# Performance work log

Measured on AMD Instinct MI355X. Metric: run time of the kernel, lower is better.

Reference implementation:

```python
import jax, jax.numpy as jnp
import numpy as np

N_NODES = 50000
N_EDGES = 800000
IN_DIM = 1024
HID = 512          # hidden_channels * heads, heads=1
N_CLASSES = 6
N_GRAPHS = 8
NEG_SLOPE = 0.2    # PyG GATConv default LeakyReLU slope
EPS = 1e-16


def gat_conv(x, W, att_src, att_dst, bias, src, dst):
    """PyG GATConv with heads=1, concat=True.
    x: [N, Fin], W: [Fin, C], att_src/att_dst: [C], bias: [C],
    src/dst: [E] (edge_index[0], edge_index[1]); messages flow src -> dst.
    """
    h = x @ W                                   # [N, C]
    a_s = h @ att_src                           # [N]
    a_d = h @ att_dst                           # [N]
    e = jax.nn.leaky_relu(a_s[src] + a_d[dst], NEG_SLOPE)   # [E]
    # segment softmax over destination node
    m = jax.ops.segment_max(e, dst, num_segments=N_NODES)   # [N]
    ex = jnp.exp(e - m[dst])                                 # [E]
    denom = jax.ops.segment_sum(ex, dst, num_segments=N_NODES)  # [N]
    alpha = ex / (denom[dst] + EPS)                           # [E]
    msg = alpha[:, None] * h[src]                             # [E, C]
    out = jax.ops.segment_sum(msg, dst, num_segments=N_NODES)  # [N, C]
    return out + bias


def setup_inputs() -> dict:
    key = jax.random.key(0)
    ks = jax.random.split(key, 20)
    x = jax.random.normal(ks[0], (N_NODES, IN_DIM), dtype=jnp.float32)
    edge_index = jax.random.randint(ks[1], (2, N_EDGES), 0, N_NODES, dtype=jnp.int32)
    batch = jnp.sort(jax.random.randint(ks[2], (N_NODES,), 0, N_GRAPHS, dtype=jnp.int32))

    def glorot(k, shape):
        fan = shape[0] + shape[-1]
        return jax.random.normal(k, shape, dtype=jnp.float32) * jnp.sqrt(2.0 / fan)

    inp = {"x": x, "edge_index": edge_index, "batch": batch}
    dims = [(IN_DIM, HID), (HID, HID), (HID, HID)]
    for i, (fi, fo) in enumerate(dims, start=1):
        inp[f"W{i}"] = glorot(ks[3 * i], (fi, fo))
        inp[f"as{i}"] = glorot(ks[3 * i + 1], (fo,))
        inp[f"ad{i}"] = glorot(ks[3 * i + 2], (fo,))
        inp[f"b{i}"] = jnp.zeros((fo,), dtype=jnp.float32)
    inp["Wlin"] = glorot(ks[13], (HID, N_CLASSES))
    inp["blin"] = jnp.zeros((N_CLASSES,), dtype=jnp.float32)
    return inp


def reference(x, W1, as1, ad1, b1, W2, as2, ad2, b2, W3, as3, ad3, b3,
              Wlin, blin, edge_index, batch):
    src, dst = edge_index[0], edge_index[1]
    h = gat_conv(x, W1, as1, ad1, b1, src, dst)
    h = jax.nn.relu(h)
    h = gat_conv(h, W2, as2, ad2, b2, src, dst)
    h = jax.nn.relu(h)
    h = gat_conv(h, W3, as3, ad3, b3, src, dst)
    # global_max_pool over graphs; dropout is identity in eval mode
    pooled = jax.ops.segment_max(h, batch, num_segments=N_GRAPHS)  # [G, HID]
    return pooled @ Wlin + blin                                     # [G, num_classes]
```

## Files before the change

### kernel.cpp

```cpp
#include <hip/hip_runtime.h>
#include <cmath>

#define N_NODES 50000
#define N_EDGES 800000
#define IN_DIM 1024
#define HID 512
#define N_CLASSES 6
#define N_GRAPHS 8
#define NEG_SLOPE 0.2f
#define SCAN_BLK 256
#define N_SCAN_BLOCKS ((N_NODES + SCAN_BLK - 1) / SCAN_BLK)
#define POOL_STRIP 256
#define POOL_NBLOCKS ((N_NODES + POOL_STRIP - 1) / POOL_STRIP)

typedef _Float16 half8 __attribute__((ext_vector_type(8)));
typedef float floatx4 __attribute__((ext_vector_type(4)));

__global__ __launch_bounds__(256) void transpose_cast_W(const float* __restrict__ W,
                                                        _Float16* __restrict__ Wt,
                                                        int K) {
    __shared__ float sh[32][33];
    const int kb = blockIdx.x * 32, nb = blockIdx.y * 32;
    const int tx = threadIdx.x & 31, ty = threadIdx.x >> 5;
#pragma unroll
    for (int i = 0; i < 32; i += 8)
        sh[ty + i][tx] = W[(size_t)(kb + ty + i) * HID + nb + tx];
    __syncthreads();
#pragma unroll
    for (int i = 0; i < 32; i += 8)
        Wt[(size_t)(nb + ty + i) * K + kb + tx] = (_Float16)sh[tx][ty + i];
}

__global__ __launch_bounds__(256) void gemm_mfma_f16(const float* __restrict__ A,
                                                     const _Float16* __restrict__ Bt,
                                                     _Float16* __restrict__ C,
                                                     int M, int K) {
    const int tid  = threadIdx.x;
    const int lane = tid & 63;
    const int wave = tid >> 6;
    const int wm = wave >> 1, wn = wave & 1;
    const int rowBase = blockIdx.y * 128;
    const int colBase = blockIdx.x * 128;

    __shared__ _Float16 As[128][40];
    __shared__ _Float16 Bs[128][40];

    const int srow  = tid >> 1;
    const int shalf = (tid & 1) * 16;

    const int fr = lane & 15;
    const int kc = lane >> 4;

    floatx4 acc[4][4] = {};

    int arow = rowBase + srow; if (arow >= M) arow = M - 1;
    const float*    aRow = A  + (size_t)arow * K + shalf;
    const _Float16* bRow = Bt + (size_t)(colBase + srow) * K + shalf;

    for (int kb = 0; kb < K; kb += 32) {
        const float* ap = aRow + kb;
        float4 af0 = *(const float4*)(ap + 0);
        float4 af1 = *(const float4*)(ap + 4);
        float4 af2 = *(const float4*)(ap + 8);
        float4 af3 = *(const float4*)(ap + 12);
        union { _Float16 h[16]; half8 v[2]; } au;
        au.h[0]  = (_Float16)af0.x; au.h[1]  = (_Float16)af0.y;
        au.h[2]  = (_Float16)af0.z; au.h[3]  = (_Float16)af0.w;
        au.h[4]  = (_Float16)af1.x; au.h[5]  = (_Float16)af1.y;
        au.h[6]  = (_Float16)af1.z; au.h[7]  = (_Float16)af1.w;
        au.h[8]  = (_Float16)af2.x; au.h[9]  = (_Float16)af2.y;
        au.h[10] = (_Float16)af2.z; au.h[11] = (_Float16)af2.w;
        au.h[12] = (_Float16)af3.x; au.h[13] = (_Float16)af3.y;
        au.h[14] = (_Float16)af3.z; au.h[15] = (_Float16)af3.w;
        half8* dstA = (half8*)&As[srow][shalf];
        const _Float16* bp = bRow + kb;
        half8 b0 = *(const half8*)bp;
        half8 b1 = *(const half8*)(bp + 8);
        half8* dstB = (half8*)&Bs[srow][shalf];
        dstA[0] = au.v[0]; dstA[1] = au.v[1];
        dstB[0] = b0;      dstB[1] = b1;
        __syncthreads();

        half8 afr[4], bfr[4];
#pragma unroll
        for (int mi = 0; mi < 4; ++mi)
            afr[mi] = *(const half8*)&As[wm * 64 + mi * 16 + fr][kc * 8];
#pragma unroll
        for (int ni = 0; ni < 4; ++ni)
            bfr[ni] = *(const half8*)&Bs[wn * 64 + ni * 16 + fr][kc * 8];
#pragma unroll
        for (int mi = 0; mi < 4; ++mi)
#pragma unroll
            for (int ni = 0; ni < 4; ++ni)
                acc[mi][ni] = __builtin_amdgcn_mfma_f32_16x16x32_f16(
                    afr[mi], bfr[ni], acc[mi][ni], 0, 0, 0);
        __syncthreads();
    }

#pragma unroll
    for (int mi = 0; mi < 4; ++mi) {
#pragma unroll
        for (int ni = 0; ni < 4; ++ni) {
            int col = colBase + wn * 64 + ni * 16 + fr;
#pragma unroll
            for (int j = 0; j < 4; ++j) {
                int row = rowBase + wm * 64 + mi * 16 + kc * 4 + j;
                if (row < M) C[(size_t)row * HID + col] = (_Float16)acc[mi][ni][j];
            }
        }
    }
}

__global__ __launch_bounds__(256) void adot_kernel(const _Float16* __restrict__ h,
                                                   const float* __restrict__ att_s,
                                                   const float* __restrict__ att_d,
                                                   float* __restrict__ a_s,
                                                   float* __restrict__ a_d) {
    int wave = threadIdx.x >> 6;
    int lane = threadIdx.x & 63;
    int n = blockIdx.x * 4 + wave;
    if (n >= N_NODES) return;
    half8 hv = *(const half8*)(h + (size_t)n * HID + lane * 8);
    float4 s0 = ((const float4*)att_s)[lane * 2];
    float4 s1 = ((const float4*)att_s)[lane * 2 + 1];
    float4 d0 = ((const float4*)att_d)[lane * 2];
    float4 d1 = ((const float4*)att_d)[lane * 2 + 1];
    float hf[8];
#pragma unroll
    for (int q = 0; q < 8; ++q) hf[q] = (float)hv[q];
    float ss = hf[0]*s0.x + hf[1]*s0.y + hf[2]*s0.z + hf[3]*s0.w
             + hf[4]*s1.x + hf[5]*s1.y + hf[6]*s1.z + hf[7]*s1.w;
    float sd = hf[0]*d0.x + hf[1]*d0.y + hf[2]*d0.z + hf[3]*d0.w
             + hf[4]*d1.x + hf[5]*d1.y + hf[6]*d1.z + hf[7]*d1.w;
#pragma unroll
    for (int off = 32; off; off >>= 1) {
        ss += __shfl_down(ss, off);
        sd += __shfl_down(sd, off);
    }
    if (lane == 0) { a_s[n] = ss; a_d[n] = sd; }
}

__global__ void count_kernel(const int* __restrict__ dst, int* __restrict__ cnt) {
    int i = blockIdx.x * blockDim.x + threadIdx.x;
    if (i < N_EDGES) atomicAdd(cnt + dst[i], 1);
}

__global__ __launch_bounds__(SCAN_BLK) void scan1_kernel(const int* __restrict__ cnt,
                                                         int* __restrict__ partial,
                                                         int* __restrict__ blocksum) {
    __shared__ int tmp[SCAN_BLK];
    int t = threadIdx.x;
    int i = blockIdx.x * SCAN_BLK + t;
    int v = (i < N_NODES) ? cnt[i] : 0;
    tmp[t] = v;
    __syncthreads();
    for (int off = 1; off < SCAN_BLK; off <<= 1) {
        int u = (t >= off) ? tmp[t - off] : 0;
        __syncthreads();
        tmp[t] += u;
        __syncthreads();
    }
    if (i < N_NODES) partial[i] = tmp[t] - v;
    if (t == SCAN_BLK - 1) blocksum[blockIdx.x] = tmp[t];
}

__global__ __launch_bounds__(SCAN_BLK) void scan2_kernel(int* __restrict__ blocksum) {
    __shared__ int tmp[SCAN_BLK];
    int t = threadIdx.x;
    int v = (t < N_SCAN_BLOCKS) ? blocksum[t] : 0;
    tmp[t] = v;
    __syncthreads();
    for (int off = 1; off < SCAN_BLK; off <<= 1) {
        int u = (t >= off) ? tmp[t - off] : 0;
        __syncthreads();
        tmp[t] += u;
        __syncthreads();
    }
    if (t < N_SCAN_BLOCKS) blocksum[t] = tmp[t] - v;
}

__global__ __launch_bounds__(SCAN_BLK) void scan3_kernel(const int* __restrict__ partial,
                                                         const int* __restrict__ blocksum,
                                                         int* __restrict__ rowptr,
                                                         int* __restrict__ cursor) {
    int i = blockIdx.x * SCAN_BLK + threadIdx.x;
    if (i < N_NODES) {
        int r = partial[i] + blocksum[blockIdx.x];
        rowptr[i] = r;
        cursor[i] = r;
    }
    if (i == 0) rowptr[N_NODES] = N_EDGES;
}

__global__ void scatter_kernel(const int* __restrict__ src, const int* __restrict__ dst,
                               int* __restrict__ cursor, int* __restrict__ src_s) {
    int i = blockIdx.x * blockDim.x + threadIdx.x;
    if (i >= N_EDGES) return;
    int p = atomicAdd(cursor + dst[i], 1);
    src_s[p] = src[i];
}

__global__ __launch_bounds__(256) void aggregate_fused(const int* __restrict__ rowptr,
                                                       const int* __restrict__ src_s,
                                                       const float* __restrict__ a_s,
                                                       const float* __restrict__ a_d,
                                                       const _Float16* __restrict__ h,
                                                       const float* __restrict__ bias,
                                                       int do_relu,
                                                       float* __restrict__ outx) {
    int wave = threadIdx.x >> 6;
    int lane = threadIdx.x & 63;
    int n = blockIdx.x * 4 + wave;
    if (n >= N_NODES) return;
    int beg = rowptr[n], end = rowptr[n + 1];
    float a_dn = a_d[n];
    float m = -__builtin_inff();
    float ssum = 0.f;
    float acc[8] = {};
    for (int j = beg; j < end; ++j) {
        int s = src_s[j];
        float v = a_s[s] + a_dn;
        v = v > 0.f ? v : NEG_SLOPE * v;
        float mn = fmaxf(m, v);
        float scale = __expf(m - mn);
        float p = __expf(v - mn);
        ssum = ssum * scale + p;
        m = mn;
        half8 hv = *(const half8*)(h + (size_t)s * HID + lane * 8);
#pragma unroll
        for (int q = 0; q < 8; ++q)
            acc[q] = fmaf(p, (float)hv[q], acc[q] * scale);
    }
    float inv = 1.f / (ssum + 1e-16f);
    const float4 b0 = ((const float4*)(bias + lane * 8))[0];
    const float4 b1 = ((const float4*)(bias + lane * 8))[1];
    float4 o0, o1;
    o0.x = acc[0] * inv + b0.x; o0.y = acc[1] * inv + b0.y;
    o0.z = acc[2] * inv + b0.z; o0.w = acc[3] * inv + b0.w;
    o1.x = acc[4] * inv + b1.x; o1.y = acc[5] * inv + b1.y;
    o1.z = acc[6] * inv + b1.z; o1.w = acc[7] * inv + b1.w;
    if (do_relu) {
        o0.x = fmaxf(o0.x, 0.f); o0.y = fmaxf(o0.y, 0.f);
        o0.z = fmaxf(o0.z, 0.f); o0.w = fmaxf(o0.w, 0.f);
        o1.x = fmaxf(o1.x, 0.f); o1.y = fmaxf(o1.y, 0.f);
        o1.z = fmaxf(o1.z, 0.f); o1.w = fmaxf(o1.w, 0.f);
    }
    float4* op = (float4*)(outx + (size_t)n * HID + lane * 8);
    op[0] = o0;
    op[1] = o1;
}

__global__ __launch_bounds__(128) void pool1_kernel(const float* __restrict__ X,
                                                    const int* __restrict__ batch,
                                                    float* __restrict__ partial) {
    const int t = threadIdx.x;
    const int b = blockIdx.x;
    const int n0 = b * POOL_STRIP;
    const int n1 = min(n0 + POOL_STRIP, N_NODES);
    const float NEG = -__builtin_inff();
    const float4 neg4 = make_float4(NEG, NEG, NEG, NEG);
#pragma unroll
    for (int g = 0; g < N_GRAPHS; ++g)
        ((float4*)(partial + ((size_t)b * N_GRAPHS + g) * HID))[t] = neg4;
    int gcur = batch[n0];
    float4 m = neg4;
    for (int n = n0; n < n1; ++n) {
        int g = batch[n];
        if (g != gcur) {
            ((float4*)(partial + ((size_t)b * N_GRAPHS + gcur) * HID))[t] = m;
            m = neg4;
            gcur = g;
        }
        float4 v = ((const float4*)(X + (size_t)n * HID))[t];
        m.x = fmaxf(m.x, v.x); m.y = fmaxf(m.y, v.y);
        m.z = fmaxf(m.z, v.z); m.w = fmaxf(m.w, v.w);
    }
    ((float4*)(partial + ((size_t)b * N_GRAPHS + gcur) * HID))[t] = m;
}

__global__ __launch_bounds__(128) void pool2_kernel(const float* __restrict__ partial,
                                                    float* __restrict__ pooled) {
    const int g = blockIdx.x;
    const int t = threadIdx.x;
    const float NEG = -__builtin_inff();
    float4 m = make_float4(NEG, NEG, NEG, NEG);
    for (int b = 0; b < POOL_NBLOCKS; ++b) {
        float4 v = ((const float4*)(partial + ((size_t)b * N_GRAPHS + g) * HID))[t];
        m.x = fmaxf(m.x, v.x); m.y = fmaxf(m.y, v.y);
        m.z = fmaxf(m.z, v.z); m.w = fmaxf(m.w, v.w);
    }
    ((float4*)(pooled + (size_t)g * HID))[t] = m;
}

__global__ __launch_bounds__(64) void final_linear_kernel(const float* __restrict__ pooled,
                                                          const float* __restrict__ Wlin,
                                                          const float* __restrict__ blin,
                                                          float* __restrict__ out) {
    int t = threadIdx.x;
    if (t >= N_GRAPHS * N_CLASSES) return;
    int g = t / N_CLASSES, c = t % N_CLASSES;
    float s = blin[c];
    for (int k = 0; k < HID; ++k)
        s = fmaf(pooled[(size_t)g * HID + k], Wlin[(size_t)k * N_CLASSES + c], s);
    out[t] = s;
}

extern "C" void kernel_launch(void* const* d_in, const int* in_sizes, int n_in,
                              void* d_out, int out_size, void* d_ws, size_t ws_size,
                              hipStream_t stream) {
    const float* x       = (const float*)d_in[0];
    const int*   eidx    = (const int*)d_in[1];
    const int*   batch   = (const int*)d_in[2];
    const float* W[3]    = {(const float*)d_in[3], (const float*)d_in[7], (const float*)d_in[11]};
    const float* Asrc[3] = {(const float*)d_in[4], (const float*)d_in[8], (const float*)d_in[12]};
    const float* Adst[3] = {(const float*)d_in[5], (const float*)d_in[9], (const float*)d_in[13]};
    const float* Bias[3] = {(const float*)d_in[6], (const float*)d_in[10], (const float*)d_in[14]};
    const float* Wlin    = (const float*)d_in[15];
    const float* blin    = (const float*)d_in[16];
    const int* src = eidx;
    const int* dst = eidx + N_EDGES;

    float* bufH   = (float*)d_ws;
    float* bufX   = bufH + (size_t)N_NODES * HID;
    float* a_s    = bufX + (size_t)N_NODES * HID;
    float* a_d    = a_s + N_NODES;
    float* pooled = a_d + N_NODES;
    int* cnt      = (int*)(pooled + N_GRAPHS * HID);
    int* rowptr   = cnt + N_NODES;
    int* cursor   = rowptr + N_NODES + 1;
    int* partial  = cursor + N_NODES;
    int* blocksum = partial + N_NODES;
    int* src_s    = blocksum + 256;
    _Float16* Wt  = (_Float16*)(src_s + N_EDGES);
    _Float16* hH  = (_Float16*)bufH;

    int edge_blocks = (N_EDGES + 255) / 256;

    hipMemsetAsync(cnt, 0, N_NODES * sizeof(int), stream);
    count_kernel<<<edge_blocks, 256, 0, stream>>>(dst, cnt);
    scan1_kernel<<<N_SCAN_BLOCKS, SCAN_BLK, 0, stream>>>(cnt, partial, blocksum);
    scan2_kernel<<<1, SCAN_BLK, 0, stream>>>(blocksum);
    scan3_kernel<<<N_SCAN_BLOCKS, SCAN_BLK, 0, stream>>>(partial, blocksum, rowptr, cursor);
    scatter_kernel<<<edge_blocks, 256, 0, stream>>>(src, dst, cursor, src_s);

    for (int l = 0; l < 3; ++l) {
        const float* Xin = (l == 0) ? x : bufX;
        int K = (l == 0) ? IN_DIM : HID;
        dim3 tgrid(K / 32, HID / 32);
        transpose_cast_W<<<tgrid, 256, 0, stream>>>(W[l], Wt, K);
        dim3 ggrid(HID / 128, (N_NODES + 127) / 128);
        gemm_mfma_f16<<<ggrid, 256, 0, stream>>>(Xin, Wt, hH, N_NODES, K);
        adot_kernel<<<(N_NODES + 3) / 4, 256, 0, stream>>>(hH, Asrc[l], Adst[l], a_s, a_d);
        aggregate_fused<<<(N_NODES + 3) / 4, 256, 0, stream>>>(
            rowptr, src_s, a_s, a_d, hH, Bias[l], (l < 2) ? 1 : 0, bufX);
    }

    float* pool_partial = bufH;
    pool1_kernel<<<POOL_NBLOCKS, 128, 0, stream>>>(bufX, batch, pool_partial);
    pool2_kernel<<<N_GRAPHS, 128, 0, stream>>>(pool_partial, pooled);
    final_linear_kernel<<<1, 64, 0, stream>>>(pooled, Wlin, blin, (float*)d_out);
}
```

Baseline: 958.7 us.

## Store layer activations in fp16 and remap GEMM blocks across XCDs

The aggregation kernel now writes its activations as fp16 instead of fp32. The layer-2/3 GEMMs read that fp16 directly through a templated A type, and the pooling kernel reads fp16 too. This halves activation write and read traffic and drops the per-iteration fp32-to-fp16 conversion in the later GEMMs. The GEMM also moves to a 1D grid with a block-id remap so that tiles given to the same XCD are contiguous, which is meant to improve L2 reuse of A rows. Final-layer outputs are now rounded to fp16 before max pooling, which slightly reduces precision.

```diff
diff --git a/kernel.cpp b/kernel.cpp
--- a/kernel.cpp
+++ b/kernel.cpp
@@ -14,6 +14,7 @@
 #define POOL_NBLOCKS ((N_NODES + POOL_STRIP - 1) / POOL_STRIP)
 
 typedef _Float16 half8 __attribute__((ext_vector_type(8)));
+typedef _Float16 half4 __attribute__((ext_vector_type(4)));
 typedef float floatx4 __attribute__((ext_vector_type(4)));
 
 __global__ __launch_bounds__(256) void transpose_cast_W(const float* __restrict__ W,
@@ -31,16 +32,24 @@
         Wt[(size_t)(nb + ty + i) * K + kb + tx] = (_Float16)sh[tx][ty + i];
 }
 
-__global__ __launch_bounds__(256) void gemm_mfma_f16(const float* __restrict__ A,
-                                                     const _Float16* __restrict__ Bt,
-                                                     _Float16* __restrict__ C,
-                                                     int M, int K) {
+template <typename AT>
+__global__ __launch_bounds__(256) void gemm_mfma(const AT* __restrict__ A,
+                                                 const _Float16* __restrict__ Bt,
+                                                 _Float16* __restrict__ C,
+                                                 int M, int K) {
+    const int nwg = gridDim.x;
+    const int bid = blockIdx.x;
+    const int q = nwg >> 3, r = nwg & 7;
+    const int xcd = bid & 7, local = bid >> 3;
+    const int wgid = (xcd < r) ? xcd * (q + 1) + local
+                               : r * (q + 1) + (xcd - r) * q + local;
+    const int rowBase = (wgid >> 2) * 128;
+    const int colBase = (wgid & 3) * 128;
+
     const int tid  = threadIdx.x;
     const int lane = tid & 63;
     const int wave = tid >> 6;
     const int wm = wave >> 1, wn = wave & 1;
-    const int rowBase = blockIdx.y * 128;
-    const int colBase = blockIdx.x * 128;
 
     __shared__ _Float16 As[128][40];
     __shared__ _Float16 Bs[128][40];
@@ -54,31 +63,38 @@
     floatx4 acc[4][4] = {};
 
     int arow = rowBase + srow; if (arow >= M) arow = M - 1;
-    const float*    aRow = A  + (size_t)arow * K + shalf;
+    const AT*       aRow = A  + (size_t)arow * K + shalf;
     const _Float16* bRow = Bt + (size_t)(colBase + srow) * K + shalf;
 
     for (int kb = 0; kb < K; kb += 32) {
-        const float* ap = aRow + kb;
-        float4 af0 = *(const float4*)(ap + 0);
-        float4 af1 = *(const float4*)(ap + 4);
-        float4 af2 = *(const float4*)(ap + 8);
-        float4 af3 = *(const float4*)(ap + 12);
-        union { _Float16 h[16]; half8 v[2]; } au;
-        au.h[0]  = (_Float16)af0.x; au.h[1]  = (_Float16)af0.y;
-        au.h[2]  = (_Float16)af0.z; au.h[3]  = (_Float16)af0.w;
-        au.h[4]  = (_Float16)af1.x; au.h[5]  = (_Float16)af1.y;
-        au.h[6]  = (_Float16)af1.z; au.h[7]  = (_Float16)af1.w;
-        au.h[8]  = (_Float16)af2.x; au.h[9]  = (_Float16)af2.y;
-        au.h[10] = (_Float16)af2.z; au.h[11] = (_Float16)af2.w;
-        au.h[12] = (_Float16)af3.x; au.h[13] = (_Float16)af3.y;
-        au.h[14] = (_Float16)af3.z; au.h[15] = (_Float16)af3.w;
         half8* dstA = (half8*)&As[srow][shalf];
+        half8* dstB = (half8*)&Bs[srow][shalf];
+        if constexpr (sizeof(AT) == 4) {
+            const float* ap = (const float*)aRow + kb;
+            float4 af0 = *(const float4*)(ap + 0);
+            float4 af1 = *(const float4*)(ap + 4);
+            float4 af2 = *(const float4*)(ap + 8);
+            float4 af3 = *(const float4*)(ap + 12);
+            union { _Float16 h[16]; half8 v[2]; } au;
+            au.h[0]  = (_Float16)af0.x; au.h[1]  = (_Float16)af0.y;
+            au.h[2]  = (_Float16)af0.z; au.h[3]  = (_Float16)af0.w;
+            au.h[4]  = (_Float16)af1.x; au.h[5]  = (_Float16)af1.y;
+            au.h[6]  = (_Float16)af1.z; au.h[7]  = (_Float16)af1.w;
+            au.h[8]  = (_Float16)af2.x; au.h[9]  = (_Float16)af2.y;
+            au.h[10] = (_Float16)af2.z; au.h[11] = (_Float16)af2.w;
+            au.h[12] = (_Float16)af3.x; au.h[13] = (_Float16)af3.y;
+            au.h[14] = (_Float16)af3.z; au.h[15] = (_Float16)af3.w;
+            dstA[0] = au.v[0]; dstA[1] = au.v[1];
+        } else {
+            const _Float16* ap = (const _Float16*)aRow + kb;
+            half8 a0 = *(const half8*)ap;
+            half8 a1 = *(const half8*)(ap + 8);
+            dstA[0] = a0; dstA[1] = a1;
+        }
         const _Float16* bp = bRow + kb;
         half8 b0 = *(const half8*)bp;
         half8 b1 = *(const half8*)(bp + 8);
-        half8* dstB = (half8*)&Bs[srow][shalf];
-        dstA[0] = au.v[0]; dstA[1] = au.v[1];
-        dstB[0] = b0;      dstB[1] = b1;
+        dstB[0] = b0; dstB[1] = b1;
         __syncthreads();
 
         half8 afr[4], bfr[4];
@@ -207,7 +223,7 @@
                                                        const _Float16* __restrict__ h,
                                                        const float* __restrict__ bias,
                                                        int do_relu,
-                                                       float* __restrict__ outx) {
+                                                       _Float16* __restrict__ outx) {
     int wave = threadIdx.x >> 6;
     int lane = threadIdx.x & 63;
     int n = blockIdx.x * 4 + wave;
@@ -234,23 +250,21 @@
     float inv = 1.f / (ssum + 1e-16f);
     const float4 b0 = ((const float4*)(bias + lane * 8))[0];
     const float4 b1 = ((const float4*)(bias + lane * 8))[1];
-    float4 o0, o1;
-    o0.x = acc[0] * inv + b0.x; o0.y = acc[1] * inv + b0.y;
-    o0.z = acc[2] * inv + b0.z; o0.w = acc[3] * inv + b0.w;
-    o1.x = acc[4] * inv + b1.x; o1.y = acc[5] * inv + b1.y;
-    o1.z = acc[6] * inv + b1.z; o1.w = acc[7] * inv + b1.w;
-    if (do_relu) {
-        o0.x = fmaxf(o0.x, 0.f); o0.y = fmaxf(o0.y, 0.f);
-        o0.z = fmaxf(o0.z, 0.f); o0.w = fmaxf(o0.w, 0.f);
-        o1.x = fmaxf(o1.x, 0.f); o1.y = fmaxf(o1.y, 0.f);
-        o1.z = fmaxf(o1.z, 0.f); o1.w = fmaxf(o1.w, 0.f);
-    }
-    float4* op = (float4*)(outx + (size_t)n * HID + lane * 8);
-    op[0] = o0;
-    op[1] = o1;
-}
-
-__global__ __launch_bounds__(128) void pool1_kernel(const float* __restrict__ X,
+    float o[8];
+    o[0] = acc[0] * inv + b0.x; o[1] = acc[1] * inv + b0.y;
+    o[2] = acc[2] * inv + b0.z; o[3] = acc[3] * inv + b0.w;
+    o[4] = acc[4] * inv + b1.x; o[5] = acc[5] * inv + b1.y;
+    o[6] = acc[6] * inv + b1.z; o[7] = acc[7] * inv + b1.w;
+    half8 ov;
+#pragma unroll
+    for (int q = 0; q < 8; ++q) {
+        float val = do_relu ? fmaxf(o[q], 0.f) : o[q];
+        ov[q] = (_Float16)val;
+    }
+    *(half8*)(outx + (size_t)n * HID + lane * 8) = ov;
+}
+
+__global__ __launch_bounds__(128) void pool1_kernel(const _Float16* __restrict__ X,
                                                     const int* __restrict__ batch,
                                                     float* __restrict__ partial) {
     const int t = threadIdx.x;
@@ -271,9 +285,9 @@
             m = neg4;
             gcur = g;
         }
-        float4 v = ((const float4*)(X + (size_t)n * HID))[t];
-        m.x = fmaxf(m.x, v.x); m.y = fmaxf(m.y, v.y);
-        m.z = fmaxf(m.z, v.z); m.w = fmaxf(m.w, v.w);
+        half4 hv = *(const half4*)(X + (size_t)n * HID + t * 4);
+        m.x = fmaxf(m.x, (float)hv[0]); m.y = fmaxf(m.y, (float)hv[1]);
+        m.z = fmaxf(m.z, (float)hv[2]); m.w = fmaxf(m.w, (float)hv[3]);
     }
     ((float4*)(partial + ((size_t)b * N_GRAPHS + gcur) * HID))[t] = m;
 }
@@ -333,6 +347,7 @@
     int* src_s    = blocksum + 256;
     _Float16* Wt  = (_Float16*)(src_s + N_EDGES);
     _Float16* hH  = (_Float16*)bufH;
+    _Float16* xAct= (_Float16*)bufX;
 
     int edge_blocks = (N_EDGES + 255) / 256;
 
@@ -343,20 +358,23 @@
     scan3_kernel<<<N_SCAN_BLOCKS, SCAN_BLK, 0, stream>>>(partial, blocksum, rowptr, cursor);
     scatter_kernel<<<edge_blocks, 256, 0, stream>>>(src, dst, cursor, src_s);
 
+    const int nrow_tiles = (N_NODES + 127) / 128;
+    const int gemm_blocks = nrow_tiles * (HID / 128);
     for (int l = 0; l < 3; ++l) {
-        const float* Xin = (l == 0) ? x : bufX;
         int K = (l == 0) ? IN_DIM : HID;
         dim3 tgrid(K / 32, HID / 32);
         transpose_cast_W<<<tgrid, 256, 0, stream>>>(W[l], Wt, K);
-        dim3 ggrid(HID / 128, (N_NODES + 127) / 128);
-        gemm_mfma_f16<<<ggrid, 256, 0, stream>>>(Xin, Wt, hH, N_NODES, K);
+        if (l == 0)
+            gemm_mfma<float><<<gemm_blocks, 256, 0, stream>>>(x, Wt, hH, N_NODES, K);
+        else
+            gemm_mfma<_Float16><<<gemm_blocks, 256, 0, stream>>>(xAct, Wt, hH, N_NODES, K);
         adot_kernel<<<(N_NODES + 3) / 4, 256, 0, stream>>>(hH, Asrc[l], Adst[l], a_s, a_d);
         aggregate_fused<<<(N_NODES + 3) / 4, 256, 0, stream>>>(
-            rowptr, src_s, a_s, a_d, hH, Bias[l], (l < 2) ? 1 : 0, bufX);
+            rowptr, src_s, a_s, a_d, hH, Bias[l], (l < 2) ? 1 : 0, xAct);
     }
 
     float* pool_partial = bufH;
-    pool1_kernel<<<POOL_NBLOCKS, 128, 0, stream>>>(bufX, batch, pool_partial);
+    pool1_kernel<<<POOL_NBLOCKS, 128, 0, stream>>>(xAct, batch, pool_partial);
     pool2_kernel<<<N_GRAPHS, 128, 0, stream>>>(pool_partial, pooled);
     final_linear_kernel<<<1, 64, 0, stream>>>(pooled, Wlin, blin, (float*)d_out);
 }
```

Measured after the change: 881.2 us. 1.09x faster.
